# Kernel optimization log

Hardware: AMD Instinct MI355X
Metric: run time of the kernel (lower is better)

## Reference

```python
import jax, jax.numpy as jnp
import numpy as np

H, D = 6, 64          # num_heads, head_dim (embed_dim = 384)
WIN = 33              # window_size
PAD = (WIN - 1) // 2  # 16


def setup_inputs() -> dict:
    key = jax.random.key(0)
    ks = jax.random.split(key, 9)
    B, L, E = 8, 1025, 384
    s = 1.0 / np.sqrt(E).astype(np.float32)
    return {
        "x": jax.random.normal(ks[0], (B, L, E), jnp.float32),
        "Wq": jax.random.normal(ks[1], (E, E), jnp.float32) * s,
        "bq": jax.random.normal(ks[2], (E,), jnp.float32) * 0.01,
        "Wk": jax.random.normal(ks[3], (E, E), jnp.float32) * s,
        "bk": jax.random.normal(ks[4], (E,), jnp.float32) * 0.01,
        "Wv": jax.random.normal(ks[5], (E, E), jnp.float32) * s,
        "bv": jax.random.normal(ks[6], (E,), jnp.float32) * 0.01,
        "Wo": jax.random.normal(ks[7], (E, E), jnp.float32) * s,
        "bo": jax.random.normal(ks[8], (E,), jnp.float32) * 0.01,
    }


def reference(x, Wq, bq, Wk, bk, Wv, bv, Wo, bo):
    B, L, E = x.shape
    scale = 1.0 / np.sqrt(D).astype(np.float32)

    def proj(W, b):
        # (B,L,E) -> (B,H,L,D)
        return (x @ W + b).reshape(B, L, H, D).transpose(0, 2, 1, 3)

    Q, K, V = proj(Wq, bq), proj(Wk, bk), proj(Wv, bv)

    # --- cls token (position 0): full attention over all keys ---
    s_cls = jnp.einsum('bhqd,bhkd->bhqk', Q[:, :, :1], K) * scale
    out_cls = jnp.einsum('bhqk,bhkd->bhqd', jax.nn.softmax(s_cls, -1), V)

    # --- remaining tokens: local window + cls appended to every window ---
    Lr = L - 1
    pos = jnp.arange(1, L)                                    # absolute query pos (Lr,)
    idx = pos[:, None] + jnp.arange(WIN)[None, :] - PAD
    # original masks out-of-range AND the cls slot (abs pos 0) inside the window
    valid = (idx >= 1) & (idx < L)
    idxc = jnp.clip(idx, 0, L - 1)

    Kw = K[:, :, idxc]
    Vw = V[:, :, idxc]
    cls_k = jnp.broadcast_to(K[:, :, :1, None, :], (B, H, Lr, 1, D))
    cls_v = jnp.broadcast_to(V[:, :, :1, None, :], (B, H, Lr, 1, D))
    Kw = jnp.concatenate([Kw, cls_k], axis=3)
    Vw = jnp.concatenate([Vw, cls_v], axis=3)
    mask = jnp.concatenate([valid, jnp.ones((Lr, 1), bool)], axis=-1)

    s_rest = jnp.einsum('bhld,bhlwd->bhlw', Q[:, :, 1:], Kw) * scale
    s_rest = jnp.where(mask[None, None], s_rest, -jnp.inf)
    a_rest = jax.nn.softmax(s_rest, axis=-1)
    out_rest = jnp.einsum('bhlw,bhlwd->bhld', a_rest, Vw)

    out = jnp.concatenate([out_cls, out_rest], axis=2)        # (B,H,L,D)
    out = out.transpose(0, 2, 1, 3).reshape(B, L, E)
    return out @ Wo + bo
```

## Files before the change

kernel.cpp:

```cpp
#include <hip/hip_runtime.h>
#include <hip/hip_bf16.h>

typedef unsigned short ushort_t;
typedef __attribute__((ext_vector_type(8))) short short8;
typedef __attribute__((ext_vector_type(4))) float f32x4;

constexpr int Bc = 8;
constexpr int Lc = 1025;
constexpr int Ec = 384;
constexpr int Hc = 6;
constexpr int Dc = 64;
constexpr int MT = Bc * Lc;
constexpr int BHLD = Bc * Hc * Lc * Dc;
constexpr float SCALE = 0.125f;
constexpr int NCH = 5;

__device__ __forceinline__ float bf2f(ushort_t u) {
    union { unsigned int u; float f; } v; v.u = ((unsigned int)u) << 16; return v.f;
}
__device__ __forceinline__ ushort_t f2bf(float f) {
    union { float f; unsigned int u; } v; v.f = f;
    unsigned int r = v.u + 0x7FFFu + ((v.u >> 16) & 1u);
    return (ushort_t)(r >> 16);
}

#define GLOAD_LDS16(gp, lp)                                                          \
    __builtin_amdgcn_global_load_lds(                                                \
        (const __attribute__((address_space(1))) unsigned int*)(gp),                 \
        (__attribute__((address_space(3))) unsigned int*)(lp), 16, 0, 0)

__global__ __launch_bounds__(256) void prep_kernel(
    const float* __restrict__ x, ushort_t* __restrict__ xb,
    const float* __restrict__ Wq, const float* __restrict__ Wk,
    const float* __restrict__ Wv, const float* __restrict__ Wo,
    ushort_t* __restrict__ Wt_all)
{
    const int bid = blockIdx.x;
    if (bid < 3075) {
        int i = bid * 256 + threadIdx.x;
        float4 v = ((const float4*)x)[i];
        ushort4 o;
        o.x = f2bf(v.x); o.y = f2bf(v.y); o.z = f2bf(v.z); o.w = f2bf(v.w);
        ((ushort4*)xb)[i] = o;
        return;
    }
    __shared__ float t[32][33];
    const int b2 = bid - 3075;
    const int z = b2 / 144, rem = b2 - z * 144;
    const int yy = rem / 12, xx = rem - yy * 12;
    const float* W = (z == 0) ? Wq : (z == 1) ? Wk : (z == 2) ? Wv : Wo;
    ushort_t* Wt = Wt_all + (size_t)z * Ec * Ec;
    const int x0 = xx * 32, y0 = yy * 32;
    const int tx = threadIdx.x & 31, ty = threadIdx.x >> 5;
#pragma unroll
    for (int j = 0; j < 4; j++)
        t[ty + 8 * j][tx] = W[(size_t)(y0 + ty + 8 * j) * Ec + x0 + tx];
    __syncthreads();
#pragma unroll
    for (int j = 0; j < 4; j++)
        Wt[(size_t)(x0 + ty + 8 * j) * Ec + y0 + tx] = f2bf(t[tx][ty + 8 * j]);
}

__global__ __launch_bounds__(256) void qkv_mfma_kernel(
    const ushort_t* __restrict__ xb, const ushort_t* __restrict__ Wt,
    const float* __restrict__ bq, const float* __restrict__ bk,
    const float* __restrict__ bv, ushort_t* __restrict__ qkv)
{
    __shared__ __align__(16) ushort_t As[2][128 * 64];
    __shared__ __align__(16) ushort_t Bs[2][128 * 64];

    const int tid = threadIdx.x;
    const int lane = tid & 63;
    const int wid = tid >> 6;
    const int wr = wid >> 1, wc = wid & 1;
    const int m0 = blockIdx.x * 128;
    const int n0 = blockIdx.y * 128;
    const int which = n0 / Ec;
    const int nm0 = n0 - which * Ec;
    const ushort_t* Wmat = Wt + (size_t)which * Ec * Ec;
    const float* bias = (which == 0) ? bq : (which == 1) ? bk : bv;

    f32x4 acc[4][4];
#pragma unroll
    for (int i = 0; i < 4; i++)
#pragma unroll
        for (int j = 0; j < 4; j++) acc[i][j] = (f32x4){0.f, 0.f, 0.f, 0.f};

#define QKV_STAGE(KT, BUF)                                                       \
    {                                                                            \
        _Pragma("unroll")                                                        \
        for (int c = 0; c < 4; c++) {                                            \
            int ci  = (wid * 4 + c) * 64 + lane;                                 \
            int row = ci >> 3, kc = ci & 7;                                      \
            int kcs = kc ^ (row & 7);                                            \
            int rowA = m0 + row; rowA = rowA < MT ? rowA : MT - 1;               \
            GLOAD_LDS16(xb + (size_t)rowA * Ec + (KT) + kcs * 8,                 \
                        As[BUF] + (size_t)(wid * 4 + c) * 512);                  \
            GLOAD_LDS16(Wmat + (size_t)(nm0 + row) * Ec + (KT) + kcs * 8,        \
                        Bs[BUF] + (size_t)(wid * 4 + c) * 512);                  \
        }                                                                        \
    }

    QKV_STAGE(0, 0);
    QKV_STAGE(64, 1);

    for (int t = 0; t < 6; ++t) {
        const int cb = t & 1;
        if (t < 5) { asm volatile("s_waitcnt vmcnt(8)" ::: "memory"); }
        else       { asm volatile("s_waitcnt vmcnt(0)" ::: "memory"); }
        __builtin_amdgcn_sched_barrier(0);
        __builtin_amdgcn_s_barrier();

        short8 a[2][4], b[2][4];
#pragma unroll
        for (int ki = 0; ki < 2; ki++) {
            const int kchunk = ki * 4 + (lane >> 4);
#pragma unroll
            for (int mi = 0; mi < 4; mi++) {
                int row = wr * 64 + mi * 16 + (lane & 15);
                a[ki][mi] = *(const short8*)(As[cb] + row * 64 + ((kchunk ^ (row & 7)) * 8));
            }
#pragma unroll
            for (int ni = 0; ni < 4; ni++) {
                int row = wc * 64 + ni * 16 + (lane & 15);
                b[ki][ni] = *(const short8*)(Bs[cb] + row * 64 + ((kchunk ^ (row & 7)) * 8));
            }
        }
        asm volatile("s_waitcnt lgkmcnt(0)" ::: "memory");
        __builtin_amdgcn_sched_barrier(0);
        __builtin_amdgcn_s_barrier();

        if (t + 2 < 6) QKV_STAGE((t + 2) * 64, cb);

#pragma unroll
        for (int ki = 0; ki < 2; ki++)
#pragma unroll
            for (int mi = 0; mi < 4; mi++)
#pragma unroll
                for (int ni = 0; ni < 4; ni++)
                    acc[mi][ni] = __builtin_amdgcn_mfma_f32_16x16x32_bf16(
                        a[ki][mi], b[ki][ni], acc[mi][ni], 0, 0, 0);
    }
#undef QKV_STAGE

    const int colL = lane & 15;
    const int rowL = (lane >> 4) * 4;
#pragma unroll
    for (int ni = 0; ni < 4; ni++) {
        int nm = nm0 + wc * 64 + ni * 16 + colL;
        float bv_ = bias[nm];
        int h = nm >> 6, d = nm & 63;
#pragma unroll
        for (int mi = 0; mi < 4; mi++) {
#pragma unroll
            for (int r = 0; r < 4; r++) {
                int m = m0 + wr * 64 + mi * 16 + rowL + r;
                if (m < MT) {
                    int b_ = m / Lc, l = m - b_ * Lc;
                    qkv[(size_t)which * BHLD +
                        ((size_t)(b_ * Hc + h) * Lc + l) * Dc + d] =
                        f2bf(acc[mi][ni][r] + bv_);
                }
            }
        }
    }
}

__global__ __launch_bounds__(256) void cls_part_kernel(
    const ushort_t* __restrict__ qkv, float* __restrict__ part)
{
    const int bh = blockIdx.x, ch = blockIdx.y;
    const int base = ch * 256;
    const int count = min(256, Lc - base);
    const ushort_t* Q = qkv + (size_t)bh * Lc * Dc;
    const ushort_t* K = Q + (size_t)BHLD;
    const ushort_t* V = Q + 2 * (size_t)BHLD;

    __shared__ float qs[64];
    __shared__ float ps[256];
    __shared__ float red[256];

    const int tid = threadIdx.x;
    if (tid < 64) qs[tid] = bf2f(Q[tid]);
    __syncthreads();

    float s = -1e30f;
    if (tid < count) {
        const ushort4* kp = (const ushort4*)(K + (size_t)(base + tid) * Dc);
        float acc = 0.f;
#pragma unroll
        for (int c = 0; c < 16; c++) {
            ushort4 kv = kp[c];
            acc += qs[c * 4 + 0] * bf2f(kv.x) + qs[c * 4 + 1] * bf2f(kv.y) +
                   qs[c * 4 + 2] * bf2f(kv.z) + qs[c * 4 + 3] * bf2f(kv.w);
        }
        s = acc * SCALE;
    }
    red[tid] = s; __syncthreads();
    for (int off = 128; off > 0; off >>= 1) {
        if (tid < off) red[tid] = fmaxf(red[tid], red[tid + off]);
        __syncthreads();
    }
    const float m = red[0];
    __syncthreads();

    float p = (tid < count) ? __expf(s - m) : 0.f;
    ps[tid] = p;
    red[tid] = p; __syncthreads();
    for (int off = 128; off > 0; off >>= 1) {
        if (tid < off) red[tid] += red[tid + off];
        __syncthreads();
    }
    const float S = red[0];
    __syncthreads();

    const int d = tid & 63, sl = tid >> 6;
    float acc = 0.f;
    for (int i = sl; i < count; i += 4)
        acc += ps[i] * bf2f(V[(size_t)(base + i) * Dc + d]);
    red[tid] = acc; __syncthreads();
    if (tid < 64) {
        float o = red[tid] + red[tid + 64] + red[tid + 128] + red[tid + 192];
        float* pp = part + (size_t)(bh * NCH + ch) * 66;
        pp[2 + tid] = o;
        if (tid == 0) { pp[0] = m; pp[1] = S; }
    }
}

__global__ __launch_bounds__(256) void win_attn_kernel(
    const ushort_t* __restrict__ qkv, const float* __restrict__ part,
    ushort_t* __restrict__ attnb)
{
    __shared__ __align__(16) ushort_t Kb[128 * 64];
    __shared__ __align__(16) ushort_t Vb[64 * 128];
    __shared__ __align__(16) ushort_t QP[64 * 128];

    const int bh = blockIdx.y;
    const int tid = threadIdx.x, lane = tid & 63, wid = tid >> 6;
    const int b_ = bh / Hc, h = bh - b_ * Hc;

    if (blockIdx.x == 16) {
        if (tid >= 64) return;
        float M = -1e30f;
#pragma unroll
        for (int ch = 0; ch < NCH; ch++)
            M = fmaxf(M, part[(size_t)(bh * NCH + ch) * 66]);
        float S = 0.f, O = 0.f;
#pragma unroll
        for (int ch = 0; ch < NCH; ch++) {
            const float* pp = part + (size_t)(bh * NCH + ch) * 66;
            float w = __expf(pp[0] - M);
            S += pp[1] * w;
            O += pp[2 + tid] * w;
        }
        attnb[(size_t)(b_ * Lc) * Ec + h * 64 + tid] = f2bf(O / S);
        return;
    }

    const int t = blockIdx.x;
    const int l0 = 1 + t * 64;
    const int k0n = l0 - 16;
    const ushort_t* Qg = qkv + (size_t)bh * Lc * Dc;
    const ushort_t* Kg = Qg + (size_t)BHLD;
    const ushort_t* Vg = Qg + 2 * (size_t)BHLD;

    short8 vreg[4];
    int vrow[4], vdc[4];
#pragma unroll
    for (int i = 0; i < 4; i++) {
        int ci = i * 256 + tid;
        if (ci < 896) {
            int j = ci >> 3, dc = ci & 7;
            int kp = (j <= 95) ? min(max(k0n + j, 0), 1024) : 0;
            vreg[i] = *(const short8*)(Vg + (size_t)kp * Dc + dc * 8);
            vrow[i] = j; vdc[i] = dc;
        } else { vrow[i] = -1; vdc[i] = 0; }
    }

#pragma unroll
    for (int i = 0; i < 4; i++) {
        int wchunk = i * 4 + wid;
        if (wchunk < 14) {
            int p = wchunk * 64 + lane;
            int j = p >> 3, c = p & 7, g = c ^ (j & 7);
            int kp = (j <= 95) ? min(max(k0n + j, 0), 1024) : 0;
            GLOAD_LDS16(Kg + (size_t)kp * Dc + g * 8,
                        Kb + (size_t)wchunk * 512);
        }
    }
#pragma unroll
    for (int i = 0; i < 2; i++) {
        int p = (i * 4 + wid) * 64 + lane;
        int q = p >> 3, c = p & 7, g = c ^ (q & 7);
        GLOAD_LDS16(Qg + (size_t)(l0 + q) * Dc + g * 8,
                    QP + (size_t)(i * 4 + wid) * 512);
    }

#pragma unroll
    for (int i = 0; i < 4; i++) {
        if (vrow[i] >= 0) {
            int j = vrow[i], jc3 = j >> 3, j7 = j & 7;
#pragma unroll
            for (int z = 0; z < 8; z++) {
                int d = vdc[i] * 8 + z;
                Vb[d * 128 + ((jc3 ^ (d & 15)) * 8) + j7] = (ushort_t)vreg[i][z];
            }
        }
    }
    if (tid < 128) {
        int d = tid >> 1, lcn = 14 + (tid & 1);
        *(short8*)(Vb + d * 128 + ((lcn ^ (d & 15)) * 8)) =
            (short8){0, 0, 0, 0, 0, 0, 0, 0};
    }
    __syncthreads();

    f32x4 sacc[7];
#pragma unroll
    for (int tj = 0; tj < 7; tj++) sacc[tj] = (f32x4){0.f, 0.f, 0.f, 0.f};
#pragma unroll
    for (int ki = 0; ki < 2; ki++) {
        const int gc = ki * 4 + (lane >> 4);
        const int qrow = wid * 16 + (lane & 15);
        short8 a = *(const short8*)(QP + qrow * 64 + ((gc ^ (qrow & 7)) * 8));
#pragma unroll
        for (int tj = 0; tj < 7; tj++) {
            int jrow = tj * 16 + (lane & 15);
            short8 b = *(const short8*)(Kb + jrow * 64 + ((gc ^ (jrow & 7)) * 8));
            sacc[tj] = __builtin_amdgcn_mfma_f32_16x16x32_bf16(a, b, sacc[tj], 0, 0, 0);
        }
    }
    __syncthreads();

    const int qb = wid * 16 + (lane >> 4) * 4;
    const int cl = lane & 15;
    float inv[4];
#pragma unroll
    for (int r = 0; r < 4; r++) {
        const int q = qb + r;
        float sv[7];
        float mx = -1e30f;
#pragma unroll
        for (int tj = 0; tj < 7; tj++) {
            int j = tj * 16 + cl;
            int kp = k0n + j;
            bool valid = (j == 96) ||
                         ((j >= q) && (j <= q + 32) && (kp >= 1) && (kp <= 1024));
            float s = valid ? sacc[tj][r] * SCALE : -1e30f;
            sv[tj] = s;
            mx = fmaxf(mx, s);
        }
        mx = fmaxf(mx, __shfl_xor(mx, 1));
        mx = fmaxf(mx, __shfl_xor(mx, 2));
        mx = fmaxf(mx, __shfl_xor(mx, 4));
        mx = fmaxf(mx, __shfl_xor(mx, 8));
        float sum = 0.f;
#pragma unroll
        for (int tj = 0; tj < 7; tj++) {
            float pv = __expf(sv[tj] - mx);
            sv[tj] = pv;
            sum += pv;
        }
        sum += __shfl_xor(sum, 1);
        sum += __shfl_xor(sum, 2);
        sum += __shfl_xor(sum, 4);
        sum += __shfl_xor(sum, 8);
        inv[r] = 1.f / sum;
#pragma unroll
        for (int tj = 0; tj < 7; tj++) {
            int j = tj * 16 + cl;
            QP[q * 128 + (((j >> 3) ^ (q & 15)) * 8) + (j & 7)] = f2bf(sv[tj]);
        }
    }
    if (cl == 0) {
#pragma unroll
        for (int r = 0; r < 4; r++) {
            int q = qb + r;
            *(short8*)(QP + q * 128 + ((14 ^ (q & 15)) * 8)) =
                (short8){0, 0, 0, 0, 0, 0, 0, 0};
            *(short8*)(QP + q * 128 + ((15 ^ (q & 15)) * 8)) =
                (short8){0, 0, 0, 0, 0, 0, 0, 0};
        }
    }
    __syncthreads();

    f32x4 oacc[4];
#pragma unroll
    for (int dt = 0; dt < 4; dt++) oacc[dt] = (f32x4){0.f, 0.f, 0.f, 0.f};
#pragma unroll
    for (int kc = 0; kc < 4; kc++) {
        const int gc = kc * 4 + (lane >> 4);
        const int qrow = wid * 16 + (lane & 15);
        short8 pa = *(const short8*)(QP + qrow * 128 + ((gc ^ (qrow & 15)) * 8));
#pragma unroll
        for (int dt = 0; dt < 4; dt++) {
            int drow = dt * 16 + (lane & 15);
            short8 vb = *(const short8*)(Vb + drow * 128 + ((gc ^ (drow & 15)) * 8));
            oacc[dt] = __builtin_amdgcn_mfma_f32_16x16x32_bf16(pa, vb, oacc[dt], 0, 0, 0);
        }
    }

#pragma unroll
    for (int dt = 0; dt < 4; dt++) {
        int d = dt * 16 + cl;
#pragma unroll
        for (int r = 0; r < 4; r++) {
            int l = l0 + qb + r;
            attnb[(size_t)(b_ * Lc + l) * Ec + h * 64 + d] = f2bf(oacc[dt][r] * inv[r]);
        }
    }
}

__global__ __launch_bounds__(256) void out_mfma_kernel(
    const ushort_t* __restrict__ attn_rows, const ushort_t* __restrict__ Wot,
    const float* __restrict__ bo, float* __restrict__ out)
{
    __shared__ __align__(16) ushort_t As[2][64 * 64];
    __shared__ __align__(16) ushort_t Bs[2][128 * 64];

    const int tid = threadIdx.x;
    const int lane = tid & 63;
    const int wid = tid >> 6;
    const int wr = wid & 1, wc = wid >> 1;
    const int m0 = blockIdx.x * 64;
    const int n0 = blockIdx.y * 128;

    f32x4 acc[2][4];
#pragma unroll
    for (int i = 0; i < 2; i++)
#pragma unroll
        for (int j = 0; j < 4; j++) acc[i][j] = (f32x4){0.f, 0.f, 0.f, 0.f};

#define OUT_STAGE(KT, BUF)                                                       \
    {                                                                            \
        _Pragma("unroll")                                                        \
        for (int c = 0; c < 2; c++) {                                            \
            int ci  = (wid * 2 + c) * 64 + lane;                                 \
            int row = ci >> 3, kc = ci & 7;                                      \
            int kcs = kc ^ (row & 7);                                            \
            int rowA = m0 + row; rowA = rowA < MT ? rowA : MT - 1;               \
            GLOAD_LDS16(attn_rows + (size_t)rowA * Ec + (KT) + kcs * 8,          \
                        As[BUF] + (size_t)(wid * 2 + c) * 512);                  \
        }                                                                        \
        _Pragma("unroll")                                                        \
        for (int c = 0; c < 4; c++) {                                            \
            int ci  = (wid * 4 + c) * 64 + lane;                                 \
            int row = ci >> 3, kc = ci & 7;                                      \
            int kcs = kc ^ (row & 7);                                            \
            GLOAD_LDS16(Wot + (size_t)(n0 + row) * Ec + (KT) + kcs * 8,          \
                        Bs[BUF] + (size_t)(wid * 4 + c) * 512);                  \
        }                                                                        \
    }

    OUT_STAGE(0, 0);
    OUT_STAGE(64, 1);

    for (int t = 0; t < 6; ++t) {
        const int cb = t & 1;
        if (t < 5) { asm volatile("s_waitcnt vmcnt(6)" ::: "memory"); }
        else       { asm volatile("s_waitcnt vmcnt(0)" ::: "memory"); }
        __builtin_amdgcn_sched_barrier(0);
        __builtin_amdgcn_s_barrier();

        short8 a[2][2], b[2][4];
#pragma unroll
        for (int ki = 0; ki < 2; ki++) {
            const int kchunk = ki * 4 + (lane >> 4);
#pragma unroll
            for (int mi = 0; mi < 2; mi++) {
                int row = wr * 32 + mi * 16 + (lane & 15);
                a[ki][mi] = *(const short8*)(As[cb] + row * 64 + ((kchunk ^ (row & 7)) * 8));
            }
#pragma unroll
            for (int ni = 0; ni < 4; ni++) {
                int row = wc * 64 + ni * 16 + (lane & 15);
                b[ki][ni] = *(const short8*)(Bs[cb] + row * 64 + ((kchunk ^ (row & 7)) * 8));
            }
        }
        asm volatile("s_waitcnt lgkmcnt(0)" ::: "memory");
        __builtin_amdgcn_sched_barrier(0);
        __builtin_amdgcn_s_barrier();

        if (t + 2 < 6) OUT_STAGE((t + 2) * 64, cb);

#pragma unroll
        for (int ki = 0; ki < 2; ki++)
#pragma unroll
            for (int mi = 0; mi < 2; mi++)
#pragma unroll
                for (int ni = 0; ni < 4; ni++)
                    acc[mi][ni] = __builtin_amdgcn_mfma_f32_16x16x32_bf16(
                        a[ki][mi], b[ki][ni], acc[mi][ni], 0, 0, 0);
    }
#undef OUT_STAGE

    const int colL = lane & 15;
    const int rowL = (lane >> 4) * 4;
#pragma unroll
    for (int ni = 0; ni < 4; ni++) {
        int n = n0 + wc * 64 + ni * 16 + colL;
        float bo_v = bo[n];
#pragma unroll
        for (int mi = 0; mi < 2; mi++) {
#pragma unroll
            for (int r = 0; r < 4; r++) {
                int m = m0 + wr * 32 + mi * 16 + rowL + r;
                if (m < MT) out[(size_t)m * Ec + n] = acc[mi][ni][r] + bo_v;
            }
        }
    }
}

extern "C" void kernel_launch(void* const* d_in, const int* in_sizes, int n_in,
                              void* d_out, int out_size, void* d_ws, size_t ws_size,
                              hipStream_t stream)
{
    const float* x  = (const float*)d_in[0];
    const float* Wq = (const float*)d_in[1];
    const float* bq = (const float*)d_in[2];
    const float* Wk = (const float*)d_in[3];
    const float* bk = (const float*)d_in[4];
    const float* Wv = (const float*)d_in[5];
    const float* bv = (const float*)d_in[6];
    const float* Wo = (const float*)d_in[7];
    const float* bo = (const float*)d_in[8];
    float* out = (float*)d_out;

    ushort_t* xb    = (ushort_t*)d_ws;
    ushort_t* Wt    = xb + (size_t)MT * Ec;
    ushort_t* qkvb  = Wt + (size_t)4 * Ec * Ec;
    ushort_t* attnb = qkvb + (size_t)3 * BHLD;
    float* clsp     = (float*)(attnb + (size_t)MT * Ec);

    prep_kernel<<<3075 + 576, 256, 0, stream>>>(x, xb, Wq, Wk, Wv, Wo, Wt);

    qkv_mfma_kernel<<<dim3((MT + 127) / 128, 9), 256, 0, stream>>>(
        xb, Wt, bq, bk, bv, qkvb);

    cls_part_kernel<<<dim3(Bc * Hc, NCH), 256, 0, stream>>>(qkvb, clsp);

    win_attn_kernel<<<dim3(17, Bc * Hc), 256, 0, stream>>>(qkvb, clsp, attnb);

    out_mfma_kernel<<<dim3((MT + 63) / 64, 3), 256, 0, stream>>>(
        attnb, Wt + (size_t)3 * Ec * Ec, bo, out);
}
```

Measured before the change: 160.3 us.

## Keep full 64-row activation tile resident in LDS across all QKV column strips

The QKV projection kernel now loads a 64x384 bf16 slab of x into shared memory once and then streams the weight matrix in 128x64 tiles through a double buffer. It loops over three 128-column strips, writing each strip's output with bias before moving on. This removes the repeated reloading of x that happened when each block computed only one 128x128 output tile over 9 column blocks. In exchange, blocks become smaller in M (64 rows) with fewer accumulators, LDS use grows to about 80KB which lowers occupancy, and the grid changes to 129x3 blocks.

```diff
diff --git a/kernel.cpp b/kernel.cpp
--- a/kernel.cpp
+++ b/kernel.cpp
@@ -66,104 +66,118 @@
     const float* __restrict__ bq, const float* __restrict__ bk,
     const float* __restrict__ bv, ushort_t* __restrict__ qkv)
 {
-    __shared__ __align__(16) ushort_t As[2][128 * 64];
-    __shared__ __align__(16) ushort_t Bs[2][128 * 64];
+    __shared__ __align__(16) ushort_t Asm[64 * 384];
+    __shared__ __align__(16) ushort_t Bsm[2][128 * 64];
 
     const int tid = threadIdx.x;
     const int lane = tid & 63;
     const int wid = tid >> 6;
-    const int wr = wid >> 1, wc = wid & 1;
-    const int m0 = blockIdx.x * 128;
-    const int n0 = blockIdx.y * 128;
-    const int which = n0 / Ec;
-    const int nm0 = n0 - which * Ec;
+    const int wr = wid & 1, wc = wid >> 1;
+    const int m0 = blockIdx.x * 64;
+    const int which = blockIdx.y;
     const ushort_t* Wmat = Wt + (size_t)which * Ec * Ec;
     const float* bias = (which == 0) ? bq : (which == 1) ? bk : bv;
-
-    f32x4 acc[4][4];
-#pragma unroll
-    for (int i = 0; i < 4; i++)
-#pragma unroll
-        for (int j = 0; j < 4; j++) acc[i][j] = (f32x4){0.f, 0.f, 0.f, 0.f};
-
-#define QKV_STAGE(KT, BUF)                                                       \
+    ushort_t* outp = qkv + (size_t)which * BHLD;
+
+#pragma unroll
+    for (int i = 0; i < 12; i++) {
+        int wchunk = wid * 12 + i;
+        int ci = wchunk * 64 + lane;
+        int row = ci / 48, c = ci - row * 48;
+        int cg = (c & ~7) | ((c & 7) ^ (row & 7));
+        int rowA = m0 + row; rowA = rowA < MT ? rowA : MT - 1;
+        GLOAD_LDS16(xb + (size_t)rowA * Ec + cg * 8,
+                    Asm + (size_t)wchunk * 512);
+    }
+
+#define B_STAGE(S, BUF)                                                          \
     {                                                                            \
+        int ns_ = (S) / 6, kt_ = (S) - ns_ * 6;                                  \
         _Pragma("unroll")                                                        \
         for (int c = 0; c < 4; c++) {                                            \
             int ci  = (wid * 4 + c) * 64 + lane;                                 \
             int row = ci >> 3, kc = ci & 7;                                      \
             int kcs = kc ^ (row & 7);                                            \
-            int rowA = m0 + row; rowA = rowA < MT ? rowA : MT - 1;               \
-            GLOAD_LDS16(xb + (size_t)rowA * Ec + (KT) + kcs * 8,                 \
-                        As[BUF] + (size_t)(wid * 4 + c) * 512);                  \
-            GLOAD_LDS16(Wmat + (size_t)(nm0 + row) * Ec + (KT) + kcs * 8,        \
-                        Bs[BUF] + (size_t)(wid * 4 + c) * 512);                  \
+            GLOAD_LDS16(Wmat + (size_t)(ns_ * 128 + row) * Ec + kt_ * 64 + kcs * 8, \
+                        Bsm[BUF] + (size_t)(wid * 4 + c) * 512);                 \
         }                                                                        \
     }
 
-    QKV_STAGE(0, 0);
-    QKV_STAGE(64, 1);
-
-    for (int t = 0; t < 6; ++t) {
-        const int cb = t & 1;
-        if (t < 5) { asm volatile("s_waitcnt vmcnt(8)" ::: "memory"); }
-        else       { asm volatile("s_waitcnt vmcnt(0)" ::: "memory"); }
+    B_STAGE(0, 0);
+    B_STAGE(1, 1);
+
+    f32x4 acc[2][4];
+#pragma unroll
+    for (int i = 0; i < 2; i++)
+#pragma unroll
+        for (int j = 0; j < 4; j++) acc[i][j] = (f32x4){0.f, 0.f, 0.f, 0.f};
+
+    const int colL = lane & 15;
+    const int rowL = (lane >> 4) * 4;
+
+    for (int s = 0; s < 18; ++s) {
+        const int cb = s & 1;
+        const int ns = s / 6, kt = s - ns * 6;
+        if (s < 17) { asm volatile("s_waitcnt vmcnt(4)" ::: "memory"); }
+        else        { asm volatile("s_waitcnt vmcnt(0)" ::: "memory"); }
         __builtin_amdgcn_sched_barrier(0);
         __builtin_amdgcn_s_barrier();
 
-        short8 a[2][4], b[2][4];
+        short8 a[2][2], b[2][4];
 #pragma unroll
         for (int ki = 0; ki < 2; ki++) {
-            const int kchunk = ki * 4 + (lane >> 4);
-#pragma unroll
-            for (int mi = 0; mi < 4; mi++) {
-                int row = wr * 64 + mi * 16 + (lane & 15);
-                a[ki][mi] = *(const short8*)(As[cb] + row * 64 + ((kchunk ^ (row & 7)) * 8));
+            const int kc = ki * 4 + (lane >> 4);
+#pragma unroll
+            for (int mi = 0; mi < 2; mi++) {
+                int row = wr * 32 + mi * 16 + (lane & 15);
+                a[ki][mi] = *(const short8*)(
+                    Asm + row * 384 + (kt * 8 + (kc ^ (row & 7))) * 8);
             }
 #pragma unroll
             for (int ni = 0; ni < 4; ni++) {
                 int row = wc * 64 + ni * 16 + (lane & 15);
-                b[ki][ni] = *(const short8*)(Bs[cb] + row * 64 + ((kchunk ^ (row & 7)) * 8));
+                b[ki][ni] = *(const short8*)(
+                    Bsm[cb] + row * 64 + ((kc ^ (row & 7)) * 8));
             }
         }
         asm volatile("s_waitcnt lgkmcnt(0)" ::: "memory");
         __builtin_amdgcn_sched_barrier(0);
         __builtin_amdgcn_s_barrier();
 
-        if (t + 2 < 6) QKV_STAGE((t + 2) * 64, cb);
+        if (s + 2 < 18) B_STAGE(s + 2, cb);
 
 #pragma unroll
         for (int ki = 0; ki < 2; ki++)
 #pragma unroll
-            for (int mi = 0; mi < 4; mi++)
+            for (int mi = 0; mi < 2; mi++)
 #pragma unroll
                 for (int ni = 0; ni < 4; ni++)
                     acc[mi][ni] = __builtin_amdgcn_mfma_f32_16x16x32_bf16(
                         a[ki][mi], b[ki][ni], acc[mi][ni], 0, 0, 0);
-    }
-#undef QKV_STAGE
-
-    const int colL = lane & 15;
-    const int rowL = (lane >> 4) * 4;
-#pragma unroll
-    for (int ni = 0; ni < 4; ni++) {
-        int nm = nm0 + wc * 64 + ni * 16 + colL;
-        float bv_ = bias[nm];
-        int h = nm >> 6, d = nm & 63;
-#pragma unroll
-        for (int mi = 0; mi < 4; mi++) {
-#pragma unroll
-            for (int r = 0; r < 4; r++) {
-                int m = m0 + wr * 64 + mi * 16 + rowL + r;
-                if (m < MT) {
-                    int b_ = m / Lc, l = m - b_ * Lc;
-                    qkv[(size_t)which * BHLD +
-                        ((size_t)(b_ * Hc + h) * Lc + l) * Dc + d] =
-                        f2bf(acc[mi][ni][r] + bv_);
+
+        if (kt == 5) {
+#pragma unroll
+            for (int ni = 0; ni < 4; ni++) {
+                int nm = ns * 128 + wc * 64 + ni * 16 + colL;
+                float bv_ = bias[nm];
+                int h = nm >> 6, d = nm & 63;
+#pragma unroll
+                for (int mi = 0; mi < 2; mi++) {
+#pragma unroll
+                    for (int r = 0; r < 4; r++) {
+                        int m = m0 + wr * 32 + mi * 16 + rowL + r;
+                        if (m < MT) {
+                            int b_ = m / Lc, l = m - b_ * Lc;
+                            outp[((size_t)(b_ * Hc + h) * Lc + l) * Dc + d] =
+                                f2bf(acc[mi][ni][r] + bv_);
+                        }
+                    }
+                    acc[mi][ni] = (f32x4){0.f, 0.f, 0.f, 0.f};
                 }
             }
         }
     }
+#undef B_STAGE
 }
 
 __global__ __launch_bounds__(256) void cls_part_kernel(
@@ -533,7 +547,7 @@
 
     prep_kernel<<<3075 + 576, 256, 0, stream>>>(x, xb, Wq, Wk, Wv, Wo, Wt);
 
-    qkv_mfma_kernel<<<dim3((MT + 127) / 128, 9), 256, 0, stream>>>(
+    qkv_mfma_kernel<<<dim3((MT + 63) / 64, 3), 256, 0, stream>>>(
         xb, Wt, bq, bk, bv, qkvb);
 
     cls_part_kernel<<<dim3(Bc * Hc, NCH), 256, 0, stream>>>(qkvb, clsp);
```

After: 160.3 us. No clear change (+0.0%).
